# Kernel tuning notes

Hardware: AMD Instinct MI355X
Metric: run time of the kernel (lower is better)

## Reference

```python
import jax, jax.numpy as jnp
import numpy as np

N_NODES = 50000
N_EDGES = 400000
F_IN = 256
HID = 64
N_CLS = 32
HEADS = 8
NEG_SLOPE = 0.2


def setup_inputs() -> dict:
    key = jax.random.key(0)
    ks = jax.random.split(key, 12)
    x = jax.random.normal(ks[0], (N_NODES, F_IN), dtype=jnp.float32)
    edge_index = jax.random.randint(ks[1], (2, N_EDGES), 0, N_NODES, dtype=jnp.int64)

    def glorot(k, shape, fan_in):
        return jax.random.normal(k, shape, dtype=jnp.float32) / np.sqrt(fan_in)

    # layer 1: in=F_IN, heads=HEADS, per-head dim=HID
    Wl1 = glorot(ks[2], (F_IN, HEADS * HID), F_IN)
    Wr1 = glorot(ks[3], (F_IN, HEADS * HID), F_IN)
    att1 = glorot(ks[4], (HEADS, HID), HID)
    b1 = jnp.zeros((HID,), dtype=jnp.float32)
    # layer 2: in=HID, heads=HEADS, per-head dim=N_CLS
    Wl2 = glorot(ks[5], (HID, HEADS * N_CLS), HID)
    Wr2 = glorot(ks[6], (HID, HEADS * N_CLS), HID)
    att2 = glorot(ks[7], (HEADS, N_CLS), N_CLS)
    b2 = jnp.zeros((N_CLS,), dtype=jnp.float32)
    # residual linear
    Wlin = glorot(ks[8], (F_IN, N_CLS), F_IN)
    blin = jnp.zeros((N_CLS,), dtype=jnp.float32)
    return {"x": x, "edge_index": edge_index,
            "Wl1": Wl1, "Wr1": Wr1, "att1": att1, "b1": b1,
            "Wl2": Wl2, "Wr2": Wr2, "att2": att2, "b2": b2,
            "Wlin": Wlin, "blin": blin}


def _gatv2(h, src, dst, Wl, Wr, att, b, n_nodes):
    """GATv2Conv, heads concat=False (head-mean). src/dst: [E] edge endpoints."""
    H, C = att.shape
    xl = (h @ Wl).reshape(n_nodes, H, C)  # source transform
    xr = (h @ Wr).reshape(n_nodes, H, C)  # target transform
    # per-edge attention logit: a . leaky_relu(x_l[src] + x_r[dst])
    e = jax.nn.leaky_relu(xl[src] + xr[dst], NEG_SLOPE)  # [E, H, C]
    logits = jnp.einsum('ehc,hc->eh', e, att)            # [E, H]
    # segment softmax over incoming edges of each target node
    m = jax.ops.segment_max(logits, dst, num_segments=n_nodes)
    m = jnp.where(jnp.isfinite(m), m, 0.0)
    p = jnp.exp(logits - m[dst])
    denom = jax.ops.segment_sum(p, dst, num_segments=n_nodes)
    alpha = p / denom[dst]                               # [E, H]
    out = jax.ops.segment_sum(xl[src] * alpha[:, :, None], dst,
                              num_segments=n_nodes)      # [N, H, C]
    return out.mean(axis=1) + b


def reference(x, edge_index, Wl1, Wr1, att1, b1, Wl2, Wr2, att2, b2, Wlin, blin):
    n = x.shape[0]
    # PyG GATv2Conv default add_self_loops=True
    loops = jnp.arange(n, dtype=edge_index.dtype)
    src = jnp.concatenate([edge_index[0], loops])
    dst = jnp.concatenate([edge_index[1], loops])
    residual = x @ Wlin + blin
    h = jax.nn.relu(_gatv2(x, src, dst, Wl1, Wr1, att1, b1, n))
    # dropout(p=0.25) is identity in eval mode
    out = _gatv2(h, src, dst, Wl2, Wr2, att2, b2, n)
    return out + residual
```

## Files before the change

### kernel.cpp

```cpp
#include <hip/hip_runtime.h>
#include <cmath>


#define NEG_SLOPE 0.2f

typedef __attribute__((ext_vector_type(4))) float f32x4;
typedef __attribute__((ext_vector_type(2))) float f32x2;
typedef __attribute__((ext_vector_type(8))) short bf16x8;

__device__ inline unsigned short f2b(float f) {
    union { float f; unsigned u; } c; c.f = f;
    return (unsigned short)((c.u + 0x8000u) >> 16);
}
__device__ inline float b2f_lo(unsigned u) { union { unsigned i; float f; } c; c.i = u << 16; return c.f; }
__device__ inline float b2f_hi(unsigned u) { union { unsigned i; float f; } c; c.i = u & 0xffff0000u; return c.f; }

__device__ inline void cstore(float* C, size_t i, float v) { C[i] = v; }
__device__ inline void cstore(unsigned short* C, size_t i, float v) { C[i] = f2b(v); }

__device__ inline void store4(unsigned short* C, size_t idx, f32x4 v) {
    uint2 pk;
    pk.x = f2b(v[0]) | ((unsigned)f2b(v[1]) << 16);
    pk.y = f2b(v[2]) | ((unsigned)f2b(v[3]) << 16);
    *(uint2*)(C + idx) = pk;
}
__device__ inline void store4(float* C, size_t idx, f32x4 v) {
    *(f32x4*)(C + idx) = v;
}

__device__ inline void gl_lds16(const void* g, void* l) {
    __builtin_amdgcn_global_load_lds(
        (const __attribute__((address_space(1))) void*)g,
        (__attribute__((address_space(3))) void*)l, 16, 0, 0);
}

__device__ inline int swz(int c) { return (c & ~7) | ((c ^ (c >> 3)) & 7); }

template <int VPL> struct RawV;
template <> struct RawV<8> { uint4 v; };
template <> struct RawV<4> { uint2 v; };

template <int VPL>
__device__ inline RawV<VPL> load_raw(const unsigned short* __restrict__ p) {
    RawV<VPL> r;
    if constexpr (VPL == 8) r.v = *reinterpret_cast<const uint4*>(p);
    else                    r.v = *reinterpret_cast<const uint2*>(p);
    return r;
}
template <int VPL>
__device__ inline void conv2(const RawV<VPL>& r, f32x2* v) {
    const unsigned* u = (const unsigned*)&r.v;
#pragma unroll
    for (int i = 0; i < VPL / 2; i++) {
        f32x2 t; t.x = b2f_lo(u[i]); t.y = b2f_hi(u[i]);
        v[i] = t;
    }
}

__global__ void k_edge_deg(const int* __restrict__ ei, int* __restrict__ deg,
                           int E, int ET) {
    int e = blockIdx.x * blockDim.x + threadIdx.x;
    if (e >= ET) return;
    int dst = (e < E) ? ei[E + e] : (e - E);
    atomicAdd(&deg[dst], 1);
}
__global__ void k_scan1(const int* __restrict__ deg, int* __restrict__ offs,
                        int* __restrict__ sums, int n) {
    __shared__ int tmp[256];
    int tid = threadIdx.x;
    int i = blockIdx.x * 256 + tid;
    int v = (i < n) ? deg[i] : 0;
    tmp[tid] = v;
    __syncthreads();
    for (int ofs = 1; ofs < 256; ofs <<= 1) {
        int add = (tid >= ofs) ? tmp[tid - ofs] : 0;
        __syncthreads();
        tmp[tid] += add;
        __syncthreads();
    }
    if (i < n) offs[i] = tmp[tid] - v;
    if (tid == 255) sums[blockIdx.x] = tmp[255];
}
__global__ void k_scan2(int* __restrict__ sums, int nb) {
    __shared__ int tmp[256];
    int tid = threadIdx.x;
    int v = (tid < nb) ? sums[tid] : 0;
    tmp[tid] = v;
    __syncthreads();
    for (int ofs = 1; ofs < 256; ofs <<= 1) {
        int add = (tid >= ofs) ? tmp[tid - ofs] : 0;
        __syncthreads();
        tmp[tid] += add;
        __syncthreads();
    }
    if (tid < nb) sums[tid] = tmp[tid] - v;
}
__global__ void k_scan3(int* __restrict__ offs, int* __restrict__ cursor,
                        const int* __restrict__ sums, int n, int total) {
    int i = blockIdx.x * blockDim.x + threadIdx.x;
    if (i < n) {
        int v = offs[i] + sums[i >> 8];
        offs[i] = v;
        cursor[i] = v;
    }
    if (i == 0) offs[n] = total;
}

__global__ void k_conv_xw(const float* __restrict__ x, unsigned short* __restrict__ xb,
                          int n_elems, int xblocks,
                          int* __restrict__ cursor, int N, int zblocks,
                          const float* __restrict__ Wl1, const float* __restrict__ Wr1,
                          const float* __restrict__ Wl2, const float* __restrict__ Wr2,
                          const float* __restrict__ Wlin,
                          unsigned short* __restrict__ Wlr1t,
                          unsigned short* __restrict__ Wlr2t,
                          unsigned short* __restrict__ WlinT) {
    int b = blockIdx.x;
    if (b < zblocks) {
        int i = b * 256 + threadIdx.x;
        if (i < N) cursor[i] = 0;
        return;
    }
    b -= zblocks;
    if (b < xblocks) {
        int i = (b * 256 + threadIdx.x) * 8;
        uint4 pk;
        if (i < n_elems) {
            float4 f0 = *(const float4*)(x + i);
            float4 f1 = *(const float4*)(x + i + 4);
            pk.x = f2b(f0.x) | ((unsigned)f2b(f0.y) << 16);
            pk.y = f2b(f0.z) | ((unsigned)f2b(f0.w) << 16);
            pk.z = f2b(f1.x) | ((unsigned)f2b(f1.y) << 16);
            pk.w = f2b(f1.z) | ((unsigned)f2b(f1.w) << 16);
        } else {
            pk = uint4{0, 0, 0, 0};
        }
        *(uint4*)(xb + i) = pk;
        return;
    }
    int i = (b - xblocks) * 256 + threadIdx.x;
    if (i < 1024 * 256) {
        int n = i >> 8, k = i & 255;
        float v = (n < 512) ? Wl1[k * 512 + n] : Wr1[k * 512 + (n - 512)];
        Wlr1t[i] = f2b(v);
        return;
    }
    i -= 1024 * 256;
    if (i < 512 * 64) {
        int n = i >> 6, k = i & 63;
        float v = (n < 256) ? Wl2[k * 256 + n] : Wr2[k * 256 + (n - 256)];
        Wlr2t[i] = f2b(v);
        return;
    }
    i -= 512 * 64;
    if (i < 128 * 256) {
        int n = i >> 8, k = i & 255;
        WlinT[i] = (n < 32) ? f2b(Wlin[k * 32 + n]) : (unsigned short)0;
    }
}

template <typename CT>
__device__ inline void mfma_body(const unsigned short* __restrict__ A,
                                 const unsigned short* __restrict__ Bt,
                                 const float* __restrict__ bias,
                                 CT* __restrict__ C1, CT* __restrict__ C2, int csplit,
                                 int Mreal, int Mout, int Nc, int K,
                                 int mt, int gx, int bid,
                                 unsigned short* As, unsigned short* Bs) {
    int xcd = bid & 7, j = bid >> 3;
    int rpx = (mt + 7) >> 3;
    int row_t = xcd * rpx + j / gx;
    int col_t = j % gx;
    if (row_t >= mt) return;
    int row0 = row_t * 128, col0 = col_t * 128;

    int tid = threadIdx.x;
    int lane = tid & 63, wid = tid >> 6;
    int wm = (wid & 1) * 64, wn = (wid >> 1) * 64;
    f32x4 acc[4][4] = {};

    for (int k0 = 0; k0 < K; k0 += 64) {
#pragma unroll
        for (int it = 0; it < 4; it++) {
            int p = tid + it * 256;
            int l = swz(p);
            int r = l >> 3, kc = (l & 7) * 8;
            int gr = row0 + r; if (gr > Mreal - 1) gr = Mreal - 1;
            gl_lds16(A + (size_t)gr * K + k0 + kc, &As[p * 8]);
            gl_lds16(Bt + (size_t)(col0 + r) * K + k0 + kc, &Bs[p * 8]);
        }
        __syncthreads();
#pragma unroll
        for (int kh = 0; kh < 2; kh++) {
            bf16x8 af[4], bfv[4];
#pragma unroll
            for (int mi = 0; mi < 4; mi++) {
                int l = (wm + mi * 16 + (lane & 15)) * 8 + kh * 4 + (lane >> 4);
                af[mi] = *(const bf16x8*)&As[swz(l) * 8];
            }
#pragma unroll
            for (int ni = 0; ni < 4; ni++) {
                int l = (wn + ni * 16 + (lane & 15)) * 8 + kh * 4 + (lane >> 4);
                bfv[ni] = *(const bf16x8*)&Bs[swz(l) * 8];
            }
#pragma unroll
            for (int mi = 0; mi < 4; mi++)
#pragma unroll
                for (int ni = 0; ni < 4; ni++)
                    acc[mi][ni] = __builtin_amdgcn_mfma_f32_16x16x32_bf16(
                        bfv[ni], af[mi], acc[mi][ni], 0, 0, 0);
        }
        __syncthreads();
    }
    CT* Cb; int cstride, cbase;
    if (col0 < csplit) { Cb = C1; cstride = csplit;      cbase = 0; }
    else               { Cb = C2; cstride = Nc - csplit; cbase = csplit; }
    int crow = lane & 15, cquad = (lane >> 4) * 4;
#pragma unroll
    for (int mi = 0; mi < 4; mi++) {
        int grow = row0 + wm + mi * 16 + crow;
        if (grow >= Mout) continue;
#pragma unroll
        for (int ni = 0; ni < 4; ni++) {
            int gcol = col0 + wn + ni * 16 + cquad;
            if (gcol >= Nc) continue;
            f32x4 v = acc[mi][ni];
            if (bias) {
                float4 bv = *(const float4*)(bias + gcol);
                v[0] += bv.x; v[1] += bv.y; v[2] += bv.z; v[3] += bv.w;
            }
            store4(Cb, (size_t)grow * cstride + (gcol - cbase), v);
        }
    }
}

template <int C, bool RELU_OUT, bool ADD_RES, typename OutT>
__device__ inline void agg_body(const unsigned short* __restrict__ xl,
                                const unsigned short* __restrict__ xr,
                                const float* __restrict__ att, const float* __restrict__ bias,
                                const float* __restrict__ res,
                                const int* __restrict__ offs, const int* __restrict__ csr_src,
                                OutT* __restrict__ out, int n_) {
    constexpr int D = 8 * C;
    constexpr int VPL = D / 64;
    constexpr int VP2 = VPL / 2;
    int n = __builtin_amdgcn_readfirstlane(n_);
    int lane = threadIdx.x & 63;
    int base = lane * VPL;

    f32x2 xr2[VP2], at2[VP2], ac2[VP2];
    {
        RawV<VPL> rr = load_raw<VPL>(xr + (size_t)n * D + base);
        conv2<VPL>(rr, xr2);
    }
    f32x2 zero2 = {0.f, 0.f};
#pragma unroll
    for (int j = 0; j < VP2; j++) {
        f32x2 a; a.x = att[base + 2 * j]; a.y = att[base + 2 * j + 1];
        at2[j] = a;
        ac2[j] = zero2;
    }
    float lsum = 0.f;
    int e0 = __builtin_amdgcn_readfirstlane(offs[n]);
    int e1 = __builtin_amdgcn_readfirstlane(offs[n + 1]);
    int deg = e1 - e0, last = e1 - 1;
#define GSRC(t) __builtin_amdgcn_readfirstlane( \
        csr_src[__builtin_amdgcn_readfirstlane(min(t, last))])
#define GLOAD(t) load_raw<VPL>(xl + (size_t)GSRC(t) * D + base)
    RawV<VPL> r0 = GLOAD(e0);
    RawV<VPL> r1 = GLOAD(e0 + 1);
    RawV<VPL> r2 = GLOAD(e0 + 2);
    RawV<VPL> r3 = GLOAD(e0 + 3);

    auto proc = [&](const RawV<VPL>& r) {
        f32x2 xs2[VP2];
        conv2<VPL>(r, xs2);
        f32x2 part2 = zero2;
#pragma unroll
        for (int j = 0; j < VP2; j++) {
            f32x2 v = xs2[j] + xr2[j];
            f32x2 t = v * NEG_SLOPE;
            f32x2 lr; lr.x = fmaxf(v.x, t.x); lr.y = fmaxf(v.y, t.y);
            part2 += at2[j] * lr;
        }
        float partial = part2.x + part2.y;
        partial += __shfl_xor(partial, 1);
        partial += __shfl_xor(partial, 2);
        partial += __shfl_xor(partial, 4);
        float p = __expf(partial);
        lsum += p;
        f32x2 p2 = {p, p};
#pragma unroll
        for (int j = 0; j < VP2; j++) ac2[j] += p2 * xs2[j];
    };

    int q = deg >> 2, rem = deg & 3;
    int e = e0;
    for (int it = 0; it < q; it++, e += 4) {
        proc(r0); r0 = GLOAD(e + 4);
        proc(r1); r1 = GLOAD(e + 5);
        proc(r2); r2 = GLOAD(e + 6);
        proc(r3); r3 = GLOAD(e + 7);
    }
    if (rem > 0) proc(r0);
    if (rem > 1) proc(r1);
    if (rem > 2) proc(r2);
#undef GLOAD
#undef GSRC

    float inv = 1.f / lsum;
    float acc[VPL];
#pragma unroll
    for (int j = 0; j < VP2; j++) {
        acc[2 * j]     = ac2[j].x * inv;
        acc[2 * j + 1] = ac2[j].y * inv;
    }
#pragma unroll
    for (int j = 0; j < VPL; j++) {
        acc[j] += __shfl_xor(acc[j], 8);
        acc[j] += __shfl_xor(acc[j], 16);
        acc[j] += __shfl_xor(acc[j], 32);
    }
    if (lane < 8) {
#pragma unroll
        for (int j = 0; j < VPL; j++) {
            int c = lane * VPL + j;
            float v = acc[j] * 0.125f + bias[c];
            if (ADD_RES) v += res[(size_t)n * C + c];
            if (RELU_OUT) v = fmaxf(v, 0.f);
            cstore(out, (size_t)n * C + c, v);
        }
    }
}

__global__ __launch_bounds__(256)
void k_gemm1_sr(const unsigned short* __restrict__ xb,
                const unsigned short* __restrict__ Wlr1t,
                unsigned short* __restrict__ xl1, unsigned short* __restrict__ xr1,
                const unsigned short* __restrict__ WlinT,
                const float* __restrict__ blin, float* __restrict__ resid,
                const int* __restrict__ ei, int* __restrict__ cursor,
                int* __restrict__ csr, int E, int ET,
                int N, int Mp, int mt, int gb1, int gbr) {
    alignas(16) __shared__ unsigned short As[128 * 64];
    alignas(16) __shared__ unsigned short Bs[128 * 64];
    int bid = blockIdx.x;
    if (bid < gb1) {
        mfma_body<unsigned short>(xb, Wlr1t, nullptr, xl1, xr1, 512,
                                  Mp, N, 1024, 256, mt, 8, bid, As, Bs);
        return;
    }
    bid -= gb1;
    if (bid < gbr) {
        mfma_body<float>(xb, WlinT, blin, resid, resid, 32,
                         Mp, N, 32, 256, mt, 1, bid, As, Bs);
        return;
    }
    bid -= gbr;
    int e = bid * 256 + threadIdx.x;
    if (e >= ET) return;
    int src, dst;
    if (e < E) { src = ei[e]; dst = ei[E + e]; }
    else { src = dst = e - E; }
    int pos = atomicAdd(&cursor[dst], 1);
    csr[pos] = src;
}

__global__ void k_agg1(const unsigned short* __restrict__ xl1, const unsigned short* __restrict__ xr1,
                       const float* __restrict__ att1, const float* __restrict__ b1,
                       const int* __restrict__ offs, const int* __restrict__ csr,
                       unsigned short* __restrict__ h1, int N) {
    int node = (blockIdx.x * blockDim.x + threadIdx.x) >> 6;
    if (node < N)
        agg_body<64, true, false>(xl1, xr1, att1, b1, nullptr, offs, csr, h1, node);
}

__global__ __launch_bounds__(256)
void k_mfma2(const unsigned short* __restrict__ h1, const unsigned short* __restrict__ Wlr2t,
             unsigned short* __restrict__ xl2, unsigned short* __restrict__ xr2,
             int N, int mt) {
    alignas(16) __shared__ unsigned short As[128 * 64];
    alignas(16) __shared__ unsigned short Bs[128 * 64];
    mfma_body<unsigned short>(h1, Wlr2t, nullptr, xl2, xr2, 256,
                              N, N, 512, 64, mt, 4, blockIdx.x, As, Bs);
}

__global__ void k_agg2(const unsigned short* __restrict__ xl2, const unsigned short* __restrict__ xr2,
                       const float* __restrict__ att2, const float* __restrict__ b2,
                       const float* __restrict__ resid,
                       const int* __restrict__ offs, const int* __restrict__ csr,
                       float* __restrict__ out, int N) {
    int node = (blockIdx.x * blockDim.x + threadIdx.x) >> 6;
    if (node < N)
        agg_body<32, false, true>(xl2, xr2, att2, b2, resid, offs, csr, out, node);
}

extern "C" void kernel_launch(void* const* d_in, const int* in_sizes, int n_in,
                              void* d_out, int out_size, void* d_ws, size_t ws_size,
                              hipStream_t stream) {
    const float* x    = (const float*)d_in[0];
    const int* ei     = (const int*)d_in[1];
    const float* Wl1  = (const float*)d_in[2];
    const float* Wr1  = (const float*)d_in[3];
    const float* att1 = (const float*)d_in[4];
    const float* b1   = (const float*)d_in[5];
    const float* Wl2  = (const float*)d_in[6];
    const float* Wr2  = (const float*)d_in[7];
    const float* att2 = (const float*)d_in[8];
    const float* b2   = (const float*)d_in[9];
    const float* Wlin = (const float*)d_in[10];
    const float* blin = (const float*)d_in[11];
    float* out = (float*)d_out;

    const int N  = in_sizes[0] / 256;
    const int E  = in_sizes[1] / 2;
    const int ET = E + N;
    const int Mp = ((N + 127) / 128) * 128;

    size_t need = (size_t)Mp * 1024 * 2 + (size_t)Mp * 256 * 2 + (size_t)Mp * 64 * 2
                + (size_t)Mp * 32 * 4
                + 1024 * 256 * 2 + 512 * 64 * 2 + 128 * 256 * 2
                + (size_t)(N + 1) * 4 + (size_t)N * 4 + (size_t)ET * 4 + 256 * 4 + 256;
    if (ws_size < need) return;

    char* w = (char*)d_ws;
    unsigned short* xl1   = (unsigned short*)w; w += (size_t)Mp * 512 * 2;
    unsigned short* xr1   = (unsigned short*)w; w += (size_t)Mp * 512 * 2;
    unsigned short* xb    = (unsigned short*)w; w += (size_t)Mp * 256 * 2;
    unsigned short* h1    = (unsigned short*)w; w += (size_t)Mp * 64 * 2;
    float* resid          = (float*)w;          w += (size_t)Mp * 32 * 4;
    unsigned short* Wlr1t = (unsigned short*)w; w += 1024 * 256 * 2;
    unsigned short* Wlr2t = (unsigned short*)w; w += 512 * 64 * 2;
    unsigned short* WlinT = (unsigned short*)w; w += 128 * 256 * 2;
    int* offs   = (int*)w; w += (size_t)(N + 1) * 4;
    int* cursor = (int*)w; w += (size_t)N * 4;
    int* csr    = (int*)w; w += (size_t)ET * 4;
    int* sums   = (int*)w; w += 256 * 4;
    unsigned short* xl2 = xl1;
    unsigned short* xr2 = xl1 + (size_t)Mp * 256;

    int nb = (N + 255) / 256;
    int xblocks = (Mp * 256 / 8) / 256;
    int wblocks = (1024 * 256 + 512 * 64 + 128 * 256 + 255) / 256;
    k_conv_xw<<<nb + xblocks + wblocks, 256, 0, stream>>>(
        x, xb, N * 256, xblocks, cursor, N, nb,
        Wl1, Wr1, Wl2, Wr2, Wlin, Wlr1t, Wlr2t, WlinT);
    k_edge_deg<<<(ET + 255) / 256, 256, 0, stream>>>(ei, cursor, E, ET);
    k_scan1<<<nb, 256, 0, stream>>>(cursor, offs, sums, N);
    k_scan2<<<1, 256, 0, stream>>>(sums, nb);
    k_scan3<<<nb, 256, 0, stream>>>(offs, cursor, sums, N, ET);

    int mt = Mp / 128;
    int rpx = (mt + 7) / 8;
    int gb1 = 8 * rpx * 8;
    int gbr = 8 * rpx;
    int sb  = (ET + 255) / 256;
    k_gemm1_sr<<<gb1 + gbr + sb, 256, 0, stream>>>(
        xb, Wlr1t, xl1, xr1, WlinT, blin, resid,
        ei, cursor, csr, E, ET, N, Mp, mt, gb1, gbr);
    int ab = (N + 3) / 4;
    k_agg1<<<ab, 256, 0, stream>>>(xl1, xr1, att1, b1, offs, csr, h1, N);
    k_mfma2<<<8 * rpx * 4, 256, 0, stream>>>(h1, Wlr2t, xl2, xr2, N, mt);
    k_agg2<<<ab, 256, 0, stream>>>(xl2, xr2, att2, b2, resid, offs, csr, out, N);
}
```

Measured before the change: 329.5 us.

## Stage bf16 GEMM epilogue through LDS and deepen aggregation gather prefetch

```diff
diff --git a/kernel.cpp b/kernel.cpp
--- a/kernel.cpp
+++ b/kernel.cpp
@@ -18,12 +18,6 @@
 __device__ inline void cstore(float* C, size_t i, float v) { C[i] = v; }
 __device__ inline void cstore(unsigned short* C, size_t i, float v) { C[i] = f2b(v); }
 
-__device__ inline void store4(unsigned short* C, size_t idx, f32x4 v) {
-    uint2 pk;
-    pk.x = f2b(v[0]) | ((unsigned)f2b(v[1]) << 16);
-    pk.y = f2b(v[2]) | ((unsigned)f2b(v[3]) << 16);
-    *(uint2*)(C + idx) = pk;
-}
 __device__ inline void store4(float* C, size_t idx, f32x4 v) {
     *(f32x4*)(C + idx) = v;
 }
@@ -166,7 +160,9 @@
                                  CT* __restrict__ C1, CT* __restrict__ C2, int csplit,
                                  int Mreal, int Mout, int Nc, int K,
                                  int mt, int gx, int bid,
-                                 unsigned short* As, unsigned short* Bs) {
+                                 unsigned short* S) {
+    unsigned short* As = S;
+    unsigned short* Bs = S + 128 * 64;
     int xcd = bid & 7, j = bid >> 3;
     int rpx = (mt + 7) >> 3;
     int row_t = xcd * rpx + j / gx;
@@ -215,21 +211,55 @@
     CT* Cb; int cstride, cbase;
     if (col0 < csplit) { Cb = C1; cstride = csplit;      cbase = 0; }
     else               { Cb = C2; cstride = Nc - csplit; cbase = csplit; }
-    int crow = lane & 15, cquad = (lane >> 4) * 4;
-#pragma unroll
-    for (int mi = 0; mi < 4; mi++) {
-        int grow = row0 + wm + mi * 16 + crow;
-        if (grow >= Mout) continue;
-#pragma unroll
-        for (int ni = 0; ni < 4; ni++) {
-            int gcol = col0 + wn + ni * 16 + cquad;
-            if (gcol >= Nc) continue;
-            f32x4 v = acc[mi][ni];
-            if (bias) {
-                float4 bv = *(const float4*)(bias + gcol);
-                v[0] += bv.x; v[1] += bv.y; v[2] += bv.z; v[3] += bv.w;
+    int crow = lane & 15, cq = lane >> 4;
+
+    if constexpr (sizeof(CT) == 2) {
+#pragma unroll
+        for (int mi = 0; mi < 4; mi++) {
+            int row = wm + mi * 16 + crow;
+#pragma unroll
+            for (int ni = 0; ni < 4; ni++) {
+                int qc = ((wn + ni * 16) >> 2) + cq;
+                int qs = qc ^ (row & 31);
+                f32x4 v = acc[mi][ni];
+                uint2 pk;
+                pk.x = f2b(v[0]) | ((unsigned)f2b(v[1]) << 16);
+                pk.y = f2b(v[2]) | ((unsigned)f2b(v[3]) << 16);
+                *(uint2*)&S[row * 128 + qs * 4] = pk;
             }
-            store4(Cb, (size_t)grow * cstride + (gcol - cbase), v);
+        }
+        __syncthreads();
+        int row = tid >> 1, half = tid & 1;
+        int grow = row0 + row;
+        if (grow < Mout) {
+            CT* dst = Cb + (size_t)grow * cstride + (col0 - cbase) + half * 64;
+#pragma unroll
+            for (int jj = 0; jj < 8; jj++) {
+                int qc0 = half * 16 + jj * 2;
+                int qs0 = qc0 ^ (row & 31);
+                int qs1 = (qc0 + 1) ^ (row & 31);
+                uint2 a = *(uint2*)&S[row * 128 + qs0 * 4];
+                uint2 b = *(uint2*)&S[row * 128 + qs1 * 4];
+                uint4 o; o.x = a.x; o.y = a.y; o.z = b.x; o.w = b.y;
+                *(uint4*)(dst + jj * 8) = o;
+            }
+        }
+    } else {
+#pragma unroll
+        for (int mi = 0; mi < 4; mi++) {
+            int grow = row0 + wm + mi * 16 + crow;
+            if (grow >= Mout) continue;
+#pragma unroll
+            for (int ni = 0; ni < 4; ni++) {
+                int gcol = col0 + wn + ni * 16 + cq * 4;
+                if (gcol >= Nc) continue;
+                f32x4 v = acc[mi][ni];
+                if (bias) {
+                    float4 bv = *(const float4*)(bias + gcol);
+                    v[0] += bv.x; v[1] += bv.y; v[2] += bv.z; v[3] += bv.w;
+                }
+                store4(Cb, (size_t)grow * cstride + (gcol - cbase), v);
+            }
         }
     }
 }
@@ -267,10 +297,9 @@
 #define GSRC(t) __builtin_amdgcn_readfirstlane( \
         csr_src[__builtin_amdgcn_readfirstlane(min(t, last))])
 #define GLOAD(t) load_raw<VPL>(xl + (size_t)GSRC(t) * D + base)
-    RawV<VPL> r0 = GLOAD(e0);
-    RawV<VPL> r1 = GLOAD(e0 + 1);
-    RawV<VPL> r2 = GLOAD(e0 + 2);
-    RawV<VPL> r3 = GLOAD(e0 + 3);
+    RawV<VPL> ring[8];
+#pragma unroll
+    for (int s = 0; s < 8; s++) ring[s] = GLOAD(e0 + s);
 
     auto proc = [&](const RawV<VPL>& r) {
         f32x2 xs2[VP2];
@@ -294,17 +323,18 @@
         for (int j = 0; j < VP2; j++) ac2[j] += p2 * xs2[j];
     };
 
-    int q = deg >> 2, rem = deg & 3;
+    int q = deg >> 3, rem = deg & 7;
     int e = e0;
-    for (int it = 0; it < q; it++, e += 4) {
-        proc(r0); r0 = GLOAD(e + 4);
-        proc(r1); r1 = GLOAD(e + 5);
-        proc(r2); r2 = GLOAD(e + 6);
-        proc(r3); r3 = GLOAD(e + 7);
-    }
-    if (rem > 0) proc(r0);
-    if (rem > 1) proc(r1);
-    if (rem > 2) proc(r2);
+    for (int it = 0; it < q; it++, e += 8) {
+#pragma unroll
+        for (int s = 0; s < 8; s++) {
+            proc(ring[s]);
+            ring[s] = GLOAD(e + 8 + s);
+        }
+    }
+#pragma unroll
+    for (int s = 0; s < 8; s++)
+        if (s < rem) proc(ring[s]);
 #undef GLOAD
 #undef GSRC
 
@@ -342,18 +372,17 @@
                 const int* __restrict__ ei, int* __restrict__ cursor,
                 int* __restrict__ csr, int E, int ET,
                 int N, int Mp, int mt, int gb1, int gbr) {
-    alignas(16) __shared__ unsigned short As[128 * 64];
-    alignas(16) __shared__ unsigned short Bs[128 * 64];
+    alignas(16) __shared__ unsigned short S[128 * 128];
     int bid = blockIdx.x;
     if (bid < gb1) {
         mfma_body<unsigned short>(xb, Wlr1t, nullptr, xl1, xr1, 512,
-                                  Mp, N, 1024, 256, mt, 8, bid, As, Bs);
+                                  Mp, N, 1024, 256, mt, 8, bid, S);
         return;
     }
     bid -= gb1;
     if (bid < gbr) {
         mfma_body<float>(xb, WlinT, blin, resid, resid, 32,
-                         Mp, N, 32, 256, mt, 1, bid, As, Bs);
+                         Mp, N, 32, 256, mt, 1, bid, S);
         return;
     }
     bid -= gbr;
@@ -379,10 +408,9 @@
 void k_mfma2(const unsigned short* __restrict__ h1, const unsigned short* __restrict__ Wlr2t,
              unsigned short* __restrict__ xl2, unsigned short* __restrict__ xr2,
              int N, int mt) {
-    alignas(16) __shared__ unsigned short As[128 * 64];
-    alignas(16) __shared__ unsigned short Bs[128 * 64];
+    alignas(16) __shared__ unsigned short S[128 * 128];
     mfma_body<unsigned short>(h1, Wlr2t, nullptr, xl2, xr2, 256,
-                              N, N, 512, 64, mt, 4, blockIdx.x, As, Bs);
+                              N, N, 512, 64, mt, 4, blockIdx.x, S);
 }
 
 __global__ void k_agg2(const unsigned short* __restrict__ xl2, const unsigned short* __restrict__ xr2,
```

After: 340.9 us. 3.5% more time.
